# Kernel optimization log

Hardware: AMD Instinct MI355X
Metric: run time of the kernel (lower is better)

Reference implementation:

```python
import jax, jax.numpy as jnp
import numpy as np
from jax import lax

B, T, K = 2048, 512, 32


def _viterbi(potentials, transitions, sequence_lengths):
    # potentials: [B,T,K], transitions: [K,K], sequence_lengths: [B]
    pot_t = jnp.moveaxis(potentials, 1, 0)  # [T,B,K]
    ts = jnp.arange(1, T)
    ident = jnp.arange(K, dtype=jnp.int32)[None, :]

    def step(alpha, inp):
        pot, t = inp
        scores = alpha[:, :, None] + transitions[None]      # [B,Kprev,Kcur]
        bp = jnp.argmax(scores, axis=1).astype(jnp.int32)   # [B,K]
        new_alpha = pot + jnp.max(scores, axis=1)
        m = (t < sequence_lengths)[:, None]
        return jnp.where(m, new_alpha, alpha), jnp.where(m, bp, ident)

    alpha, bps = lax.scan(step, pot_t[0], (pot_t[1:], ts))
    best_score = jnp.max(alpha, axis=1)                      # [B]
    last_tag = jnp.argmax(alpha, axis=1).astype(jnp.int32)   # [B]

    def back(tag, bp):
        prev = jnp.take_along_axis(bp, tag[:, None], axis=1)[:, 0]
        return prev, prev

    _, tags_prefix = lax.scan(back, last_tag, bps, reverse=True)  # [T-1,B]
    tags = jnp.concatenate([tags_prefix, last_tag[None]], axis=0)  # [T,B]
    return jnp.moveaxis(tags, 0, 1), best_score


def _log_norm(potentials, transitions, sequence_lengths):
    pot_t = jnp.moveaxis(potentials, 1, 0)  # [T,B,K]
    ts = jnp.arange(1, T)

    def step(alpha, inp):
        pot, t = inp
        new = pot + jax.nn.logsumexp(alpha[:, :, None] + transitions[None], axis=1)
        return jnp.where((t < sequence_lengths)[:, None], new, alpha), None

    alpha, _ = lax.scan(step, pot_t[0], (pot_t[1:], ts))
    return jax.nn.logsumexp(alpha, axis=1)  # [B]


def _sequence_score(potentials, transitions, tag_indices, sequence_lengths):
    t_range = jnp.arange(T)
    umask = (t_range[None, :] < sequence_lengths[:, None]).astype(potentials.dtype)   # [B,T]
    unary = jnp.sum(
        jnp.take_along_axis(potentials, tag_indices[..., None].astype(jnp.int32), axis=2)[..., 0] * umask,
        axis=1,
    )
    bmask = (t_range[None, : T - 1] < (sequence_lengths - 1)[:, None]).astype(potentials.dtype)
    binary = jnp.sum(transitions[tag_indices[:, :-1], tag_indices[:, 1:]] * bmask, axis=1)
    return unary + binary


def setup_inputs() -> dict:
    key = jax.random.key(0)
    k1, k2, k3, k4 = jax.random.split(key, 4)
    potentials = jax.random.normal(k1, (B, T, K), dtype=jnp.float32)
    sequence_lengths = jax.random.randint(k2, (B,), 1, T + 1, dtype=jnp.int32)
    tag_indices = jax.random.randint(k3, (B, T), 0, K, dtype=jnp.int32)
    transitions = 0.1 * jax.random.normal(k4, (K, K), dtype=jnp.float32)
    return {
        "potentials": potentials,
        "transitions": transitions,
        "sequence_lengths": sequence_lengths,
        "tag_indices": tag_indices,
    }


def reference(potentials, transitions, sequence_lengths, tag_indices):
    decode_tags, best_score = _viterbi(potentials, transitions, sequence_lengths)
    log_norm = _log_norm(potentials, transitions, sequence_lengths)
    seq_score = _sequence_score(potentials, transitions, tag_indices, sequence_lengths)
    log_likelihood = seq_score - log_norm
    return decode_tags, best_score, log_likelihood
```

## Files before the change

### kernel.cpp

```cpp
#include <hip/hip_runtime.h>

#define BB 2048
#define TT 512
#define KK 32

#define VBLK(q, t0, t1, t2, t3, base, m, bi) do {                       \
    float s0_ = (q).x + (t0), s1_ = (q).y + (t1);                       \
    float s2_ = (q).z + (t2), s3_ = (q).w + (t3);                       \
    m = s0_; bi = (base);                                               \
    if (s1_ > m) { m = s1_; bi = (base) + 1; }                          \
    if (s2_ > m) { m = s2_; bi = (base) + 2; }                          \
    if (s3_ > m) { m = s3_; bi = (base) + 3; }                          \
} while (0)

#define VSTEPF(T, PR) do {                                              \
    float nl_ = pot[min((T) + 8, last) * KK + j];                       \
    s_a[j] = alpha;                                                     \
    __builtin_amdgcn_wave_barrier();                                    \
    const float4 q0 = *(const float4*)(s_a + i0);                       \
    const float4 q1 = *(const float4*)(s_a + i0 + 4);                   \
    const float4 q2 = *(const float4*)(s_a + i0 + 8);                   \
    const float4 q3 = *(const float4*)(s_a + i0 + 12);                  \
    float m0, m1, m2, m3; int b0, b1, b2, b3;                           \
    VBLK(q0, tA[0],  tA[1],  tA[2],  tA[3],  i0 + 0,  m0, b0);          \
    VBLK(q1, tA[4],  tA[5],  tA[6],  tA[7],  i0 + 4,  m1, b1);          \
    VBLK(q2, tA[8],  tA[9],  tA[10], tA[11], i0 + 8,  m2, b2);          \
    VBLK(q3, tA[12], tA[13], tA[14], tA[15], i0 + 12, m3, b3);          \
    if (m1 > m0) { m0 = m1; b0 = b1; }                                  \
    if (m3 > m2) { m2 = m3; b2 = b3; }                                  \
    if (m2 > m0) { m0 = m2; b0 = b2; }                                  \
    float om = __shfl_xor(m0, 32, 64);                                  \
    int   ob = __shfl_xor(b0, 32, 64);                                  \
    bool won = half ? (m0 > om) : (m0 >= om);                           \
    float mm = fmaxf(m0, om);                                           \
    int bwin_ = won ? b0 : ob;                                          \
    if (won) s_bp[(T) * KK + j] = (unsigned char)b0;                    \
    cmap = __shfl(cmap, bwin_, 64);                                     \
    if (((T) & 31) == 0) {                                              \
        s_cmF[((((T) >> 5) - 1) << 5) + j] = (unsigned char)cmap;       \
        cmap = j;                                                       \
    }                                                                   \
    alpha = PR + mm;                                                    \
    PR = nl_;                                                           \
} while (0)

#define VSTEPB(T, PR) do {                                              \
    float nl_ = pot[max((T) - 8, 0) * KK + j];                          \
    s_g[j] = gamma;                                                     \
    __builtin_amdgcn_wave_barrier();                                    \
    const float4 q0 = *(const float4*)(s_g + i0);                       \
    const float4 q1 = *(const float4*)(s_g + i0 + 4);                   \
    const float4 q2 = *(const float4*)(s_g + i0 + 8);                   \
    const float4 q3 = *(const float4*)(s_g + i0 + 12);                  \
    float m0, m1, m2, m3; int b0, b1, b2, b3;                           \
    VBLK(q0, tB[0],  tB[1],  tB[2],  tB[3],  i0 + 0,  m0, b0);          \
    VBLK(q1, tB[4],  tB[5],  tB[6],  tB[7],  i0 + 4,  m1, b1);          \
    VBLK(q2, tB[8],  tB[9],  tB[10], tB[11], i0 + 8,  m2, b2);          \
    VBLK(q3, tB[12], tB[13], tB[14], tB[15], i0 + 12, m3, b3);          \
    if (m1 > m0) { m0 = m1; b0 = b1; }                                  \
    if (m3 > m2) { m2 = m3; b2 = b3; }                                  \
    if (m2 > m0) { m0 = m2; b0 = b2; }                                  \
    float om = __shfl_xor(m0, 32, 64);                                  \
    int   ob = __shfl_xor(b0, 32, 64);                                  \
    bool won = half ? (m0 > om) : (m0 >= om);                           \
    float mm = fmaxf(m0, om);                                           \
    int bwin_ = won ? b0 : ob;                                          \
    if (won) s_bp[((T) + 1) * KK + j] = (unsigned char)b0;              \
    cmapb = __shfl(cmapb, bwin_, 64);                                   \
    if ((((T) - m) & 31) == 0) {                                        \
        s_cmB[((((T) - m) >> 5) << 5) + j] = (unsigned char)cmapb;      \
        cmapb = j;                                                      \
    }                                                                   \
    gamma = PR + mm;                                                    \
    PR = nl_;                                                           \
} while (0)

#define LSTEPF(T, PR) do {                                              \
    float nl_ = pot[min((T) + 8, last) * KK + j];                       \
    float M = __builtin_amdgcn_readfirstlane(beta);                     \
    float p = __expf(beta - M);                                         \
    s_p[j] = p;                                                         \
    __builtin_amdgcn_wave_barrier();                                    \
    const float4 q0 = *(const float4*)(s_p + i0);                       \
    const float4 q1 = *(const float4*)(s_p + i0 + 4);                   \
    const float4 q2 = *(const float4*)(s_p + i0 + 8);                   \
    const float4 q3 = *(const float4*)(s_p + i0 + 12);                  \
    float a0 = fmaf(q0.x, tE[0],  q0.y * tE[1]);                        \
    a0 = fmaf(q0.z, tE[2],  a0); a0 = fmaf(q0.w, tE[3],  a0);           \
    float a1 = fmaf(q1.x, tE[4],  q1.y * tE[5]);                        \
    a1 = fmaf(q1.z, tE[6],  a1); a1 = fmaf(q1.w, tE[7],  a1);           \
    float a2 = fmaf(q2.x, tE[8],  q2.y * tE[9]);                        \
    a2 = fmaf(q2.z, tE[10], a2); a2 = fmaf(q2.w, tE[11], a2);           \
    float a3 = fmaf(q3.x, tE[12], q3.y * tE[13]);                       \
    a3 = fmaf(q3.z, tE[14], a3); a3 = fmaf(q3.w, tE[15], a3);           \
    float ssum = (a0 + a1) + (a2 + a3);                                 \
    ssum += __shfl_xor(ssum, 32, 64);                                   \
    beta = PR + M + __logf(ssum);                                       \
    PR = nl_;                                                           \
} while (0)

#define LSTEPB(T, PR) do {                                              \
    float nl_ = pot[max((T) - 8, 0) * KK + j];                          \
    float M = __builtin_amdgcn_readfirstlane(gl);                       \
    float p = __expf(gl - M);                                           \
    s_q[j] = p;                                                         \
    __builtin_amdgcn_wave_barrier();                                    \
    const float4 q0 = *(const float4*)(s_q + i0);                       \
    const float4 q1 = *(const float4*)(s_q + i0 + 4);                   \
    const float4 q2 = *(const float4*)(s_q + i0 + 8);                   \
    const float4 q3 = *(const float4*)(s_q + i0 + 12);                  \
    float a0 = fmaf(q0.x, tEB[0],  q0.y * tEB[1]);                      \
    a0 = fmaf(q0.z, tEB[2],  a0); a0 = fmaf(q0.w, tEB[3],  a0);         \
    float a1 = fmaf(q1.x, tEB[4],  q1.y * tEB[5]);                      \
    a1 = fmaf(q1.z, tEB[6],  a1); a1 = fmaf(q1.w, tEB[7],  a1);         \
    float a2 = fmaf(q2.x, tEB[8],  q2.y * tEB[9]);                      \
    a2 = fmaf(q2.z, tEB[10], a2); a2 = fmaf(q2.w, tEB[11], a2);         \
    float a3 = fmaf(q3.x, tEB[12], q3.y * tEB[13]);                     \
    a3 = fmaf(q3.z, tEB[14], a3); a3 = fmaf(q3.w, tEB[15], a3);         \
    float ssum = (a0 + a1) + (a2 + a3);                                 \
    ssum += __shfl_xor(ssum, 32, 64);                                   \
    gl = PR + M + __logf(ssum);                                         \
    PR = nl_;                                                           \
} while (0)

__launch_bounds__(512)
__global__ void build_perm(const int* __restrict__ seqlen,
                           int* __restrict__ perm) {
    __shared__ int hist[TT + 1];
    const int tid = threadIdx.x;
    for (int i = tid; i <= TT; i += 512) hist[i] = 0;
    __syncthreads();
    for (int i = tid; i < BB; i += 512) atomicAdd(&hist[seqlen[i]], 1);
    __syncthreads();
    if (tid == 0) {
        int acc = 0;
        for (int L = TT; L >= 1; --L) { int c = hist[L]; hist[L] = acc; acc += c; }
    }
    __syncthreads();
    for (int i = tid; i < BB; i += 512) {
        int pos = atomicAdd(&hist[seqlen[i]], 1);
        perm[pos] = i;
    }
}

__launch_bounds__(256)
__global__ void crf_kernel(const float* __restrict__ pot_g,
                           const float* __restrict__ trans,
                           const int* __restrict__ seqlen,
                           const int* __restrict__ tagidx,
                           float* __restrict__ out,
                           const int* __restrict__ perm,
                           int use_perm) {
    __shared__ __align__(16) float s_a[KK];
    __shared__ __align__(16) float s_g[KK];
    __shared__ __align__(16) float s_p[KK];
    __shared__ __align__(16) float s_q[KK];
    __shared__ unsigned char s_bp[TT * KK];
    __shared__ unsigned char s_cmF[8 * KK];
    __shared__ unsigned char s_cmB[10 * KK];

    const int tid  = threadIdx.x;
    const int wv   = tid >> 6;
    const int lane = tid & 63;
    const int j    = lane & 31;
    const int half = lane >> 5;
    const int i0   = half << 4;
    const int b    = use_perm ? perm[blockIdx.x] : blockIdx.x;

    const float* pot = pot_g + (size_t)b * (TT * KK);
    const int len  = seqlen[b];
    const int last = len - 1;
    const int m = ((last + 1) >> 1) & ~31;
    float* out_tags = out + (size_t)b * TT;

    if (wv == 0) {
        float tA[16];
#pragma unroll
        for (int k = 0; k < 16; ++k) tA[k] = trans[(i0 + k) * KK + j];
        int cmap = j;
        float alpha = pot[j];
        float pr0 = pot[min(1, last) * KK + j];
        float pr1 = pot[min(2, last) * KK + j];
        float pr2 = pot[min(3, last) * KK + j];
        float pr3 = pot[min(4, last) * KK + j];
        float pr4 = pot[min(5, last) * KK + j];
        float pr5 = pot[min(6, last) * KK + j];
        float pr6 = pot[min(7, last) * KK + j];
        float pr7 = pot[min(8, last) * KK + j];
        int t = 1;
        for (; t + 7 <= m; t += 8) {
            VSTEPF(t,     pr0); VSTEPF(t + 1, pr1);
            VSTEPF(t + 2, pr2); VSTEPF(t + 3, pr3);
            VSTEPF(t + 4, pr4); VSTEPF(t + 5, pr5);
            VSTEPF(t + 6, pr6); VSTEPF(t + 7, pr7);
        }
        s_a[j] = alpha;
    } else if (wv == 1) {
        float tB[16];
#pragma unroll
        for (int k = 0; k < 16; ++k) tB[k] = trans[j * KK + i0 + k];
        int cmapb = j;
        float gamma = pot[last * KK + j];
        float pr0 = pot[max(last - 1, 0) * KK + j];
        float pr1 = pot[max(last - 2, 0) * KK + j];
        float pr2 = pot[max(last - 3, 0) * KK + j];
        float pr3 = pot[max(last - 4, 0) * KK + j];
        float pr4 = pot[max(last - 5, 0) * KK + j];
        float pr5 = pot[max(last - 6, 0) * KK + j];
        float pr6 = pot[max(last - 7, 0) * KK + j];
        float pr7 = pot[max(last - 8, 0) * KK + j];
        int t = last - 1;
        for (; t - 7 >= m; t -= 8) {
            VSTEPB(t,     pr0); VSTEPB(t - 1, pr1);
            VSTEPB(t - 2, pr2); VSTEPB(t - 3, pr3);
            VSTEPB(t - 4, pr4); VSTEPB(t - 5, pr5);
            VSTEPB(t - 6, pr6); VSTEPB(t - 7, pr7);
        }
        if (t >= m) { VSTEPB(t, pr0); --t; }
        if (t >= m) { VSTEPB(t, pr1); --t; }
        if (t >= m) { VSTEPB(t, pr2); --t; }
        if (t >= m) { VSTEPB(t, pr3); --t; }
        if (t >= m) { VSTEPB(t, pr4); --t; }
        if (t >= m) { VSTEPB(t, pr5); --t; }
        if (t >= m) { VSTEPB(t, pr6); --t; }
        s_g[j] = gamma;
    } else if (wv == 2) {
        float tE[16];
#pragma unroll
        for (int k = 0; k < 16; ++k) tE[k] = __expf(trans[(i0 + k) * KK + j]);
        const int* tagrow = tagidx + (size_t)b * TT;
        float su = 0.0f;
#pragma unroll
        for (int c = 0; c < TT / 64; ++c) {
            int tt = c * 64 + lane;
            if (tt < len) {
                int tg = tagrow[tt];
                su += pot[tt * KK + tg];
                if (tt < last) {
                    int tg2 = tagrow[tt + 1];
                    su += trans[tg * KK + tg2];
                }
            }
        }
#pragma unroll
        for (int d = 1; d < 64; d <<= 1) su += __shfl_xor(su, d, 64);
        if (lane == 0) out[(size_t)BB * TT + BB + b] = su;

        float beta = pot[j];
        float pr0 = pot[min(1, last) * KK + j];
        float pr1 = pot[min(2, last) * KK + j];
        float pr2 = pot[min(3, last) * KK + j];
        float pr3 = pot[min(4, last) * KK + j];
        float pr4 = pot[min(5, last) * KK + j];
        float pr5 = pot[min(6, last) * KK + j];
        float pr6 = pot[min(7, last) * KK + j];
        float pr7 = pot[min(8, last) * KK + j];
        int t = 1;
        for (; t + 7 <= m; t += 8) {
            LSTEPF(t,     pr0); LSTEPF(t + 1, pr1);
            LSTEPF(t + 2, pr2); LSTEPF(t + 3, pr3);
            LSTEPF(t + 4, pr4); LSTEPF(t + 5, pr5);
            LSTEPF(t + 6, pr6); LSTEPF(t + 7, pr7);
        }
        s_p[j] = beta;
    } else {
        float tEB[16];
#pragma unroll
        for (int k = 0; k < 16; ++k) tEB[k] = __expf(trans[j * KK + i0 + k]);
        float gl = pot[last * KK + j];
        float pr0 = pot[max(last - 1, 0) * KK + j];
        float pr1 = pot[max(last - 2, 0) * KK + j];
        float pr2 = pot[max(last - 3, 0) * KK + j];
        float pr3 = pot[max(last - 4, 0) * KK + j];
        float pr4 = pot[max(last - 5, 0) * KK + j];
        float pr5 = pot[max(last - 6, 0) * KK + j];
        float pr6 = pot[max(last - 7, 0) * KK + j];
        float pr7 = pot[max(last - 8, 0) * KK + j];
        int t = last - 1;
        for (; t - 7 >= m; t -= 8) {
            LSTEPB(t,     pr0); LSTEPB(t - 1, pr1);
            LSTEPB(t - 2, pr2); LSTEPB(t - 3, pr3);
            LSTEPB(t - 4, pr4); LSTEPB(t - 5, pr5);
            LSTEPB(t - 6, pr6); LSTEPB(t - 7, pr7);
        }
        if (t >= m) { LSTEPB(t, pr0); --t; }
        if (t >= m) { LSTEPB(t, pr1); --t; }
        if (t >= m) { LSTEPB(t, pr2); --t; }
        if (t >= m) { LSTEPB(t, pr3); --t; }
        if (t >= m) { LSTEPB(t, pr4); --t; }
        if (t >= m) { LSTEPB(t, pr5); --t; }
        if (t >= m) { LSTEPB(t, pr6); --t; }
        s_q[j] = gl;
    }

    __syncthreads();

    if (wv == 0 || wv == 1) {
        float v = s_a[j] + s_g[j] - pot[m * KK + j];
        float bv = v; int bj = j;
#pragma unroll
        for (int d = 1; d < 32; d <<= 1) {
            float ov = __shfl_xor(bv, d, 64);
            int   oj = __shfl_xor(bj, d, 64);
            if (ov > bv || (ov == bv && oj < bj)) { bv = ov; bj = oj; }
        }
        if (wv == 0) {
            if (lane == 0) {
                out[(size_t)BB * TT + b] = bv;
                out_tags[m] = (float)bj;
            }
            const int C_f = m >> 5;
            int e = bj, my_e = bj;
            for (int c = C_f - 1; c >= 1; --c) {
                e = s_cmF[(c << 5) + e];
                if (lane == c - 1) my_e = e;
            }
            if (lane < C_f) {
                int cur = my_e;
                const int tend = (lane << 5) + 32;
#pragma unroll
                for (int r = 0; r < 32; ++r) {
                    int tt = tend - r;
                    cur = s_bp[tt * KK + cur];
                    out_tags[tt - 1] = (float)cur;
                }
            }
        } else {
            const int C_b = (last - m + 31) >> 5;
            int e = bj, my_e = bj;
            for (int c = 0; c < C_b; ++c) {
                if (lane == c) my_e = e;
                e = s_cmB[(c << 5) + e];
            }
            if (lane < C_b) {
                int cur = my_e;
                const int tlo = m + (lane << 5);
                const int thi = min(tlo + 31, last - 1);
#pragma unroll
                for (int r = 0; r < 32; ++r) {
                    int tt = tlo + r;
                    if (tt <= thi) {
                        cur = s_bp[(tt + 1) * KK + cur];
                        out_tags[tt + 1] = (float)cur;
                    }
                }
            }
            for (int tt = last + 1 + lane; tt < TT; tt += 64)
                out_tags[tt] = (float)e;
        }
    } else if (wv == 2) {
        float v = s_p[j] + s_q[j] - pot[m * KK + j];
        float Mf = v;
#pragma unroll
        for (int d = 1; d < 32; d <<= 1) Mf = fmaxf(Mf, __shfl_xor(Mf, d, 64));
        float e = __expf(v - Mf);
#pragma unroll
        for (int d = 1; d < 32; d <<= 1) e += __shfl_xor(e, d, 64);
        float ln = Mf + __logf(e);
        if (lane == 0) out[(size_t)BB * TT + BB + b] -= ln;
    }
}

extern "C" void kernel_launch(void* const* d_in, const int* in_sizes, int n_in,
                              void* d_out, int out_size, void* d_ws, size_t ws_size,
                              hipStream_t stream) {
    const float* potentials = (const float*)d_in[0];
    const float* transitions = (const float*)d_in[1];
    const int* sequence_lengths = (const int*)d_in[2];
    const int* tag_indices = (const int*)d_in[3];
    float* out = (float*)d_out;
    int* perm = (int*)d_ws;
    const int use_perm = (ws_size >= BB * sizeof(int)) ? 1 : 0;
    if (use_perm)
        build_perm<<<1, 512, 0, stream>>>(sequence_lengths, perm);
    crf_kernel<<<BB, 256, 0, stream>>>(potentials, transitions, sequence_lengths,
                                       tag_indices, out, perm, use_perm);
}
```

Before: 294.4 us.

## Fuse Viterbi and log-normalizer recurrences into two waves per block

```diff
diff --git a/kernel.cpp b/kernel.cpp
--- a/kernel.cpp
+++ b/kernel.cpp
@@ -13,14 +13,21 @@
     if (s3_ > m) { m = s3_; bi = (base) + 3; }                          \
 } while (0)
 
-#define VSTEPF(T, PR) do {                                              \
+#define FSTEP(T, PR) do {                                               \
     float nl_ = pot[min((T) + 8, last) * KK + j];                       \
     s_a[j] = alpha;                                                     \
+    float M = __builtin_amdgcn_readfirstlane(beta);                     \
+    float p_ = __expf(beta - M);                                        \
+    s_p[j] = p_;                                                        \
     __builtin_amdgcn_wave_barrier();                                    \
     const float4 q0 = *(const float4*)(s_a + i0);                       \
     const float4 q1 = *(const float4*)(s_a + i0 + 4);                   \
     const float4 q2 = *(const float4*)(s_a + i0 + 8);                   \
     const float4 q3 = *(const float4*)(s_a + i0 + 12);                  \
+    const float4 r0 = *(const float4*)(s_p + i0);                       \
+    const float4 r1 = *(const float4*)(s_p + i0 + 4);                   \
+    const float4 r2 = *(const float4*)(s_p + i0 + 8);                   \
+    const float4 r3 = *(const float4*)(s_p + i0 + 12);                  \
     float m0, m1, m2, m3; int b0, b1, b2, b3;                           \
     VBLK(q0, tA[0],  tA[1],  tA[2],  tA[3],  i0 + 0,  m0, b0);          \
     VBLK(q1, tA[4],  tA[5],  tA[6],  tA[7],  i0 + 4,  m1, b1);          \
@@ -40,18 +47,36 @@
         s_cmF[((((T) >> 5) - 1) << 5) + j] = (unsigned char)cmap;       \
         cmap = j;                                                       \
     }                                                                   \
+    float a0 = fmaf(r0.x, tE[0],  r0.y * tE[1]);                        \
+    a0 = fmaf(r0.z, tE[2],  a0); a0 = fmaf(r0.w, tE[3],  a0);           \
+    float a1 = fmaf(r1.x, tE[4],  r1.y * tE[5]);                        \
+    a1 = fmaf(r1.z, tE[6],  a1); a1 = fmaf(r1.w, tE[7],  a1);           \
+    float a2 = fmaf(r2.x, tE[8],  r2.y * tE[9]);                        \
+    a2 = fmaf(r2.z, tE[10], a2); a2 = fmaf(r2.w, tE[11], a2);           \
+    float a3 = fmaf(r3.x, tE[12], r3.y * tE[13]);                       \
+    a3 = fmaf(r3.z, tE[14], a3); a3 = fmaf(r3.w, tE[15], a3);           \
+    float ssum = (a0 + a1) + (a2 + a3);                                 \
+    ssum += __shfl_xor(ssum, 32, 64);                                   \
     alpha = PR + mm;                                                    \
+    beta  = PR + M + __logf(ssum);                                      \
     PR = nl_;                                                           \
 } while (0)
 
-#define VSTEPB(T, PR) do {                                              \
+#define BSTEP(T, PR) do {                                               \
     float nl_ = pot[max((T) - 8, 0) * KK + j];                          \
     s_g[j] = gamma;                                                     \
+    float M = __builtin_amdgcn_readfirstlane(gl);                       \
+    float p_ = __expf(gl - M);                                          \
+    s_q[j] = p_;                                                        \
     __builtin_amdgcn_wave_barrier();                                    \
     const float4 q0 = *(const float4*)(s_g + i0);                       \
     const float4 q1 = *(const float4*)(s_g + i0 + 4);                   \
     const float4 q2 = *(const float4*)(s_g + i0 + 8);                   \
     const float4 q3 = *(const float4*)(s_g + i0 + 12);                  \
+    const float4 r0 = *(const float4*)(s_q + i0);                       \
+    const float4 r1 = *(const float4*)(s_q + i0 + 4);                   \
+    const float4 r2 = *(const float4*)(s_q + i0 + 8);                   \
+    const float4 r3 = *(const float4*)(s_q + i0 + 12);                  \
     float m0, m1, m2, m3; int b0, b1, b2, b3;                           \
     VBLK(q0, tB[0],  tB[1],  tB[2],  tB[3],  i0 + 0,  m0, b0);          \
     VBLK(q1, tB[4],  tB[5],  tB[6],  tB[7],  i0 + 4,  m1, b1);          \
@@ -71,55 +96,18 @@
         s_cmB[((((T) - m) >> 5) << 5) + j] = (unsigned char)cmapb;      \
         cmapb = j;                                                      \
     }                                                                   \
-    gamma = PR + mm;                                                    \
-    PR = nl_;                                                           \
-} while (0)
-
-#define LSTEPF(T, PR) do {                                              \
-    float nl_ = pot[min((T) + 8, last) * KK + j];                       \
-    float M = __builtin_amdgcn_readfirstlane(beta);                     \
-    float p = __expf(beta - M);                                         \
-    s_p[j] = p;                                                         \
-    __builtin_amdgcn_wave_barrier();                                    \
-    const float4 q0 = *(const float4*)(s_p + i0);                       \
-    const float4 q1 = *(const float4*)(s_p + i0 + 4);                   \
-    const float4 q2 = *(const float4*)(s_p + i0 + 8);                   \
-    const float4 q3 = *(const float4*)(s_p + i0 + 12);                  \
-    float a0 = fmaf(q0.x, tE[0],  q0.y * tE[1]);                        \
-    a0 = fmaf(q0.z, tE[2],  a0); a0 = fmaf(q0.w, tE[3],  a0);           \
-    float a1 = fmaf(q1.x, tE[4],  q1.y * tE[5]);                        \
-    a1 = fmaf(q1.z, tE[6],  a1); a1 = fmaf(q1.w, tE[7],  a1);           \
-    float a2 = fmaf(q2.x, tE[8],  q2.y * tE[9]);                        \
-    a2 = fmaf(q2.z, tE[10], a2); a2 = fmaf(q2.w, tE[11], a2);           \
-    float a3 = fmaf(q3.x, tE[12], q3.y * tE[13]);                       \
-    a3 = fmaf(q3.z, tE[14], a3); a3 = fmaf(q3.w, tE[15], a3);           \
+    float a0 = fmaf(r0.x, tEB[0],  r0.y * tEB[1]);                      \
+    a0 = fmaf(r0.z, tEB[2],  a0); a0 = fmaf(r0.w, tEB[3],  a0);         \
+    float a1 = fmaf(r1.x, tEB[4],  r1.y * tEB[5]);                      \
+    a1 = fmaf(r1.z, tEB[6],  a1); a1 = fmaf(r1.w, tEB[7],  a1);         \
+    float a2 = fmaf(r2.x, tEB[8],  r2.y * tEB[9]);                      \
+    a2 = fmaf(r2.z, tEB[10], a2); a2 = fmaf(r2.w, tEB[11], a2);         \
+    float a3 = fmaf(r3.x, tEB[12], r3.y * tEB[13]);                     \
+    a3 = fmaf(r3.z, tEB[14], a3); a3 = fmaf(r3.w, tEB[15], a3);         \
     float ssum = (a0 + a1) + (a2 + a3);                                 \
     ssum += __shfl_xor(ssum, 32, 64);                                   \
-    beta = PR + M + __logf(ssum);                                       \
-    PR = nl_;                                                           \
-} while (0)
-
-#define LSTEPB(T, PR) do {                                              \
-    float nl_ = pot[max((T) - 8, 0) * KK + j];                          \
-    float M = __builtin_amdgcn_readfirstlane(gl);                       \
-    float p = __expf(gl - M);                                           \
-    s_q[j] = p;                                                         \
-    __builtin_amdgcn_wave_barrier();                                    \
-    const float4 q0 = *(const float4*)(s_q + i0);                       \
-    const float4 q1 = *(const float4*)(s_q + i0 + 4);                   \
-    const float4 q2 = *(const float4*)(s_q + i0 + 8);                   \
-    const float4 q3 = *(const float4*)(s_q + i0 + 12);                  \
-    float a0 = fmaf(q0.x, tEB[0],  q0.y * tEB[1]);                      \
-    a0 = fmaf(q0.z, tEB[2],  a0); a0 = fmaf(q0.w, tEB[3],  a0);         \
-    float a1 = fmaf(q1.x, tEB[4],  q1.y * tEB[5]);                      \
-    a1 = fmaf(q1.z, tEB[6],  a1); a1 = fmaf(q1.w, tEB[7],  a1);         \
-    float a2 = fmaf(q2.x, tEB[8],  q2.y * tEB[9]);                      \
-    a2 = fmaf(q2.z, tEB[10], a2); a2 = fmaf(q2.w, tEB[11], a2);         \
-    float a3 = fmaf(q3.x, tEB[12], q3.y * tEB[13]);                     \
-    a3 = fmaf(q3.z, tEB[14], a3); a3 = fmaf(q3.w, tEB[15], a3);         \
-    float ssum = (a0 + a1) + (a2 + a3);                                 \
-    ssum += __shfl_xor(ssum, 32, 64);                                   \
-    gl = PR + M + __logf(ssum);                                         \
+    gamma = PR + mm;                                                    \
+    gl    = PR + M + __logf(ssum);                                      \
     PR = nl_;                                                           \
 } while (0)
 
@@ -143,7 +131,7 @@
     }
 }
 
-__launch_bounds__(256)
+__launch_bounds__(128)
 __global__ void crf_kernel(const float* __restrict__ pot_g,
                            const float* __restrict__ trans,
                            const int* __restrict__ seqlen,
@@ -172,13 +160,34 @@
     const int last = len - 1;
     const int m = ((last + 1) >> 1) & ~31;
     float* out_tags = out + (size_t)b * TT;
+    float su = 0.0f;
 
     if (wv == 0) {
-        float tA[16];
-#pragma unroll
-        for (int k = 0; k < 16; ++k) tA[k] = trans[(i0 + k) * KK + j];
+        float tA[16], tE[16];
+#pragma unroll
+        for (int k = 0; k < 16; ++k) {
+            tA[k] = trans[(i0 + k) * KK + j];
+            tE[k] = __expf(tA[k]);
+        }
+        const int* tagrow = tagidx + (size_t)b * TT;
+#pragma unroll
+        for (int c = 0; c < TT / 64; ++c) {
+            int tt = c * 64 + lane;
+            if (tt < len) {
+                int tg = tagrow[tt];
+                su += pot[tt * KK + tg];
+                if (tt < last) {
+                    int tg2 = tagrow[tt + 1];
+                    su += trans[tg * KK + tg2];
+                }
+            }
+        }
+#pragma unroll
+        for (int d = 1; d < 64; d <<= 1) su += __shfl_xor(su, d, 64);
+
         int cmap = j;
         float alpha = pot[j];
+        float beta  = alpha;
         float pr0 = pot[min(1, last) * KK + j];
         float pr1 = pot[min(2, last) * KK + j];
         float pr2 = pot[min(3, last) * KK + j];
@@ -189,18 +198,23 @@
         float pr7 = pot[min(8, last) * KK + j];
         int t = 1;
         for (; t + 7 <= m; t += 8) {
-            VSTEPF(t,     pr0); VSTEPF(t + 1, pr1);
-            VSTEPF(t + 2, pr2); VSTEPF(t + 3, pr3);
-            VSTEPF(t + 4, pr4); VSTEPF(t + 5, pr5);
-            VSTEPF(t + 6, pr6); VSTEPF(t + 7, pr7);
+            FSTEP(t,     pr0); FSTEP(t + 1, pr1);
+            FSTEP(t + 2, pr2); FSTEP(t + 3, pr3);
+            FSTEP(t + 4, pr4); FSTEP(t + 5, pr5);
+            FSTEP(t + 6, pr6); FSTEP(t + 7, pr7);
         }
         s_a[j] = alpha;
-    } else if (wv == 1) {
-        float tB[16];
-#pragma unroll
-        for (int k = 0; k < 16; ++k) tB[k] = trans[j * KK + i0 + k];
+        s_p[j] = beta;
+    } else {
+        float tB[16], tEB[16];
+#pragma unroll
+        for (int k = 0; k < 16; ++k) {
+            tB[k]  = trans[j * KK + i0 + k];
+            tEB[k] = __expf(tB[k]);
+        }
         int cmapb = j;
         float gamma = pot[last * KK + j];
+        float gl    = gamma;
         float pr0 = pot[max(last - 1, 0) * KK + j];
         float pr1 = pot[max(last - 2, 0) * KK + j];
         float pr2 = pot[max(last - 3, 0) * KK + j];
@@ -211,91 +225,25 @@
         float pr7 = pot[max(last - 8, 0) * KK + j];
         int t = last - 1;
         for (; t - 7 >= m; t -= 8) {
-            VSTEPB(t,     pr0); VSTEPB(t - 1, pr1);
-            VSTEPB(t - 2, pr2); VSTEPB(t - 3, pr3);
-            VSTEPB(t - 4, pr4); VSTEPB(t - 5, pr5);
-            VSTEPB(t - 6, pr6); VSTEPB(t - 7, pr7);
-        }
-        if (t >= m) { VSTEPB(t, pr0); --t; }
-        if (t >= m) { VSTEPB(t, pr1); --t; }
-        if (t >= m) { VSTEPB(t, pr2); --t; }
-        if (t >= m) { VSTEPB(t, pr3); --t; }
-        if (t >= m) { VSTEPB(t, pr4); --t; }
-        if (t >= m) { VSTEPB(t, pr5); --t; }
-        if (t >= m) { VSTEPB(t, pr6); --t; }
+            BSTEP(t,     pr0); BSTEP(t - 1, pr1);
+            BSTEP(t - 2, pr2); BSTEP(t - 3, pr3);
+            BSTEP(t - 4, pr4); BSTEP(t - 5, pr5);
+            BSTEP(t - 6, pr6); BSTEP(t - 7, pr7);
+        }
+        if (t >= m) { BSTEP(t, pr0); --t; }
+        if (t >= m) { BSTEP(t, pr1); --t; }
+        if (t >= m) { BSTEP(t, pr2); --t; }
+        if (t >= m) { BSTEP(t, pr3); --t; }
+        if (t >= m) { BSTEP(t, pr4); --t; }
+        if (t >= m) { BSTEP(t, pr5); --t; }
+        if (t >= m) { BSTEP(t, pr6); --t; }
         s_g[j] = gamma;
-    } else if (wv == 2) {
-        float tE[16];
-#pragma unroll
-        for (int k = 0; k < 16; ++k) tE[k] = __expf(trans[(i0 + k) * KK + j]);
-        const int* tagrow = tagidx + (size_t)b * TT;
-        float su = 0.0f;
-#pragma unroll
-        for (int c = 0; c < TT / 64; ++c) {
-            int tt = c * 64 + lane;
-            if (tt < len) {
-                int tg = tagrow[tt];
-                su += pot[tt * KK + tg];
-                if (tt < last) {
-                    int tg2 = tagrow[tt + 1];
-                    su += trans[tg * KK + tg2];
-                }
-            }
-        }
-#pragma unroll
-        for (int d = 1; d < 64; d <<= 1) su += __shfl_xor(su, d, 64);
-        if (lane == 0) out[(size_t)BB * TT + BB + b] = su;
-
-        float beta = pot[j];
-        float pr0 = pot[min(1, last) * KK + j];
-        float pr1 = pot[min(2, last) * KK + j];
-        float pr2 = pot[min(3, last) * KK + j];
-        float pr3 = pot[min(4, last) * KK + j];
-        float pr4 = pot[min(5, last) * KK + j];
-        float pr5 = pot[min(6, last) * KK + j];
-        float pr6 = pot[min(7, last) * KK + j];
-        float pr7 = pot[min(8, last) * KK + j];
-        int t = 1;
-        for (; t + 7 <= m; t += 8) {
-            LSTEPF(t,     pr0); LSTEPF(t + 1, pr1);
-            LSTEPF(t + 2, pr2); LSTEPF(t + 3, pr3);
-            LSTEPF(t + 4, pr4); LSTEPF(t + 5, pr5);
-            LSTEPF(t + 6, pr6); LSTEPF(t + 7, pr7);
-        }
-        s_p[j] = beta;
-    } else {
-        float tEB[16];
-#pragma unroll
-        for (int k = 0; k < 16; ++k) tEB[k] = __expf(trans[j * KK + i0 + k]);
-        float gl = pot[last * KK + j];
-        float pr0 = pot[max(last - 1, 0) * KK + j];
-        float pr1 = pot[max(last - 2, 0) * KK + j];
-        float pr2 = pot[max(last - 3, 0) * KK + j];
-        float pr3 = pot[max(last - 4, 0) * KK + j];
-        float pr4 = pot[max(last - 5, 0) * KK + j];
-        float pr5 = pot[max(last - 6, 0) * KK + j];
-        float pr6 = pot[max(last - 7, 0) * KK + j];
-        float pr7 = pot[max(last - 8, 0) * KK + j];
-        int t = last - 1;
-        for (; t - 7 >= m; t -= 8) {
-            LSTEPB(t,     pr0); LSTEPB(t - 1, pr1);
-            LSTEPB(t - 2, pr2); LSTEPB(t - 3, pr3);
-            LSTEPB(t - 4, pr4); LSTEPB(t - 5, pr5);
-            LSTEPB(t - 6, pr6); LSTEPB(t - 7, pr7);
-        }
-        if (t >= m) { LSTEPB(t, pr0); --t; }
-        if (t >= m) { LSTEPB(t, pr1); --t; }
-        if (t >= m) { LSTEPB(t, pr2); --t; }
-        if (t >= m) { LSTEPB(t, pr3); --t; }
-        if (t >= m) { LSTEPB(t, pr4); --t; }
-        if (t >= m) { LSTEPB(t, pr5); --t; }
-        if (t >= m) { LSTEPB(t, pr6); --t; }
         s_q[j] = gl;
     }
 
     __syncthreads();
 
-    if (wv == 0 || wv == 1) {
+    {
         float v = s_a[j] + s_g[j] - pot[m * KK + j];
         float bv = v; int bj = j;
 #pragma unroll
@@ -325,6 +273,15 @@
                     out_tags[tt - 1] = (float)cur;
                 }
             }
+            float v2 = s_p[j] + s_q[j] - pot[m * KK + j];
+            float Mf = v2;
+#pragma unroll
+            for (int d = 1; d < 32; d <<= 1) Mf = fmaxf(Mf, __shfl_xor(Mf, d, 64));
+            float e2 = __expf(v2 - Mf);
+#pragma unroll
+            for (int d = 1; d < 32; d <<= 1) e2 += __shfl_xor(e2, d, 64);
+            float ln = Mf + __logf(e2);
+            if (lane == 0) out[(size_t)BB * TT + BB + b] = su - ln;
         } else {
             const int C_b = (last - m + 31) >> 5;
             int e = bj, my_e = bj;
@@ -348,16 +305,6 @@
             for (int tt = last + 1 + lane; tt < TT; tt += 64)
                 out_tags[tt] = (float)e;
         }
-    } else if (wv == 2) {
-        float v = s_p[j] + s_q[j] - pot[m * KK + j];
-        float Mf = v;
-#pragma unroll
-        for (int d = 1; d < 32; d <<= 1) Mf = fmaxf(Mf, __shfl_xor(Mf, d, 64));
-        float e = __expf(v - Mf);
-#pragma unroll
-        for (int d = 1; d < 32; d <<= 1) e += __shfl_xor(e, d, 64);
-        float ln = Mf + __logf(e);
-        if (lane == 0) out[(size_t)BB * TT + BB + b] -= ln;
     }
 }
 
@@ -373,6 +320,6 @@
     const int use_perm = (ws_size >= BB * sizeof(int)) ? 1 : 0;
     if (use_perm)
         build_perm<<<1, 512, 0, stream>>>(sequence_lengths, perm);
-    crf_kernel<<<BB, 256, 0, stream>>>(potentials, transitions, sequence_lengths,
+    crf_kernel<<<BB, 128, 0, stream>>>(potentials, transitions, sequence_lengths,
                                        tag_indices, out, perm, use_perm);
 }
```

Result: slower. 320.5 us (+8.9%).
